# Optimization experiments

Hardware: AMD Instinct MI355X
Metric: run time of the kernel (lower is better)

Reference implementation:

```python
import jax, jax.numpy as jnp
import numpy as np

B, N, S, F0, C, NOUT = 16, 64, 4, 8, 32, 1
N_VALID = 48  # valid (unpadded) nodes per graph


def setup_inputs() -> dict:
    key = jax.random.key(0)
    ks = jax.random.split(key, 12)
    valid = (jnp.arange(N) < N_VALID).astype(jnp.float32)  # [N]
    # node features, zero for padded nodes; last column is the binary mask
    x_feat = jax.random.normal(ks[0], (B, N, F0), dtype=jnp.float32) * valid[None, :, None]
    x = jnp.concatenate([x_feat, jnp.broadcast_to(valid[None, :, None], (B, N, 1))], axis=-1)
    # sparse-ish binary adjacency (avg degree ~ 0.1*N), zeroed on padded rows/cols
    a = (jax.random.uniform(ks[1], (B, N, N)) < 0.1).astype(jnp.float32)
    a = a * valid[None, :, None] * valid[None, None, :]
    # edge features, only on existing edges
    e = jax.random.normal(ks[2], (B, N, N, S), dtype=jnp.float32) * a[..., None]
    sc = 0.1
    return {
        "x": x, "a": a, "e": e,
        # ECCConv 1: F_in = F0 -> C
        "w1_kern": jax.random.normal(ks[3], (S, C * F0), dtype=jnp.float32) * sc,
        "b1_kern": jnp.zeros((C * F0,), jnp.float32),
        "w1_root": jax.random.normal(ks[4], (F0, C), dtype=jnp.float32) * sc,
        "b1": jnp.zeros((C,), jnp.float32),
        # ECCConv 2: F_in = C -> C
        "w2_kern": jax.random.normal(ks[5], (S, C * C), dtype=jnp.float32) * sc,
        "b2_kern": jnp.zeros((C * C,), jnp.float32),
        "w2_root": jax.random.normal(ks[6], (C, C), dtype=jnp.float32) * sc,
        "b2": jnp.zeros((C,), jnp.float32),
        # readout dense
        "w_dense": jax.random.normal(ks[7], (C, NOUT), dtype=jnp.float32) * sc,
        "b_dense": jnp.zeros((NOUT,), jnp.float32),
    }


def _ecc(x, a, e, wk, bk, wr, b, mask):
    # spektral ECCConv, batch mode
    Bb, Nn = x.shape[0], x.shape[1]
    Fin = x.shape[-1]
    Cc = wr.shape[1]
    # per-edge filter weights from edge features: [B,N,N,C,Fin]
    kernel = (e @ wk + bk).reshape(Bb, Nn, Nn, Cc, Fin)
    # output[b,t,c] = sum_{i,f} kernel[b,t,i,c,f] * a[b,t,i] * x[b,i,f]
    msg = jnp.einsum("btixy,bti,biy->btx", kernel, a, x)
    out = msg + x @ wr + b
    out = out * mask[..., None]  # keras mask applied before activation
    return jax.nn.relu(out)


def reference(x, a, e, w1_kern, b1_kern, w1_root, b1,
              w2_kern, b2_kern, w2_root, b2, w_dense, b_dense):
    # GraphMasking: strip last feature column, use it as node mask
    mask = x[..., -1]      # [B,N]
    h = x[..., :-1]        # [B,N,F0]
    h = _ecc(h, a, e, w1_kern, b1_kern, w1_root, b1, mask)
    h = _ecc(h, a, e, w2_kern, b2_kern, w2_root, b2, mask)
    pooled = jnp.sum(h * mask[..., None], axis=1)  # GlobalSumPool with mask -> [B,C]
    return pooled @ w_dense + b_dense              # [B, n_out]
```

## Files before the change

### kernel.cpp

```cpp
#include <hip/hip_runtime.h>
#include <hip/hip_bf16.h>

#define NT 1024

constexpr int B_ = 16, N_ = 64, S_ = 4, F0_ = 8, C_ = 32;
constexpr int MAXE = 32;

typedef __attribute__((ext_vector_type(8))) short short8;
typedef __attribute__((ext_vector_type(4))) float f32x4;

__device__ __forceinline__ unsigned short f2bf(float x) {
    __hip_bfloat16 h = __float2bfloat16(x);
    return *reinterpret_cast<unsigned short*>(&h);
}

template<int F, int LOG2F, int SFP, int KSTEPS>
__device__ __forceinline__ void ecc_layer(
    int tid, const float* hin, float* hout,
    const float* __restrict__ wk, const float* __restrict__ bk,
    const float* __restrict__ wr, const float* __restrict__ bb,
    const float4* ec4, const unsigned char* nbr_idx, const int* nbr_cnt,
    const float* mask_sh, unsigned short* u_bf, unsigned short* wT,
    float* b_sh)
{
    constexpr int SF = 6 * F;
    constexpr int KTOT = KSTEPS * 32;

    for (int idx = tid; idx < C_ * SF; idx += NT) {
        int c = idx / SF, sf = idx - c * SF;
        int s = sf / F, f = sf - s * F;
        float v;
        if (s < 4)       v = wk[(s * C_ + c) * F + f];
        else if (s == 4) v = bk[c * F + f];
        else             v = wr[f * C_ + c];
        wT[c * SFP + sf] = f2bf(v);
    }
    if (KTOT > SF) {
        constexpr int PADK = KTOT - SF;
        for (int idx = tid; idx < C_ * PADK; idx += NT) {
            int c = idx / PADK, k = idx - c * PADK;
            wT[c * SFP + SF + k] = 0;
        }
        for (int idx = tid; idx < N_ * PADK; idx += NT) {
            int t = idx / PADK, k = idx - t * PADK;
            u_bf[t * SFP + SF + k] = 0;
        }
    }
    if (tid < C_) b_sh[tid] = bb[tid];

    for (int pair = tid; pair < N_ * F; pair += NT) {
        int t = pair >> LOG2F;
        int f = pair & (F - 1);
        float u0 = 0.f, u1 = 0.f, u2 = 0.f, u3 = 0.f, u4 = 0.f;
        const int cnt = nbr_cnt[t];
        for (int j = 0; j < cnt; ++j) {
            int i = nbr_idx[t * MAXE + j];
            float hv = hin[i * F + f];
            float4 ev = ec4[t * MAXE + j];
            u0 = fmaf(ev.x, hv, u0);
            u1 = fmaf(ev.y, hv, u1);
            u2 = fmaf(ev.z, hv, u2);
            u3 = fmaf(ev.w, hv, u3);
            u4 += hv;
        }
        unsigned short* ut = u_bf + t * SFP;
        ut[0 * F + f] = f2bf(u0);
        ut[1 * F + f] = f2bf(u1);
        ut[2 * F + f] = f2bf(u2);
        ut[3 * F + f] = f2bf(u3);
        ut[4 * F + f] = f2bf(u4);
        ut[5 * F + f] = f2bf(hin[t * F + f]);
    }
    __syncthreads();

    const int wv = tid >> 6;
    if (wv < 8) {
        const int lane = tid & 63, quad = lane >> 4, l16 = lane & 15;
        const int mt = wv >> 1, nt = wv & 1;
        f32x4 acc = {0.f, 0.f, 0.f, 0.f};
        const unsigned short* arow = u_bf + (mt * 16 + l16) * SFP;
        const unsigned short* brow = wT + (nt * 16 + l16) * SFP;
#pragma unroll
        for (int kk = 0; kk < KSTEPS; ++kk) {
            const int kb = kk * 32 + quad * 8;
            short8 av = *reinterpret_cast<const short8*>(arow + kb);
            short8 bv = *reinterpret_cast<const short8*>(brow + kb);
            acc = __builtin_amdgcn_mfma_f32_16x16x32_bf16(av, bv, acc, 0, 0, 0);
        }
        const int cc = nt * 16 + l16;
        const float bc = b_sh[cc];
#pragma unroll
        for (int r = 0; r < 4; ++r) {
            const int tt = mt * 16 + quad * 4 + r;
            float v = (acc[r] + bc) * mask_sh[tt];
            hout[tt * C_ + cc] = v > 0.f ? v : 0.f;
        }
    }
    __syncthreads();
}

__global__ __launch_bounds__(NT) void ecc_fused(
    const float* __restrict__ x,  const float* __restrict__ a,  const float* __restrict__ e,
    const float* __restrict__ w1k, const float* __restrict__ b1k,
    const float* __restrict__ w1r, const float* __restrict__ b1v,
    const float* __restrict__ w2k, const float* __restrict__ b2k,
    const float* __restrict__ w2r, const float* __restrict__ b2v,
    const float* __restrict__ wd,  const float* __restrict__ bd,
    float* __restrict__ out)
{
    __shared__ float x_sh[N_ * F0_];
    __shared__ float mask_sh[N_];
    __shared__ float h_sh[N_ * C_];
    __shared__ __align__(16) unsigned short u_bf[N_ * 200];
    __shared__ __align__(16) unsigned short wT_bf[C_ * 200];
    __shared__ __align__(16) float4 ec4[N_ * MAXE];
    __shared__ unsigned char nbr_idx[N_ * MAXE];
    __shared__ int nbr_cnt[N_];
    __shared__ float b_sh[C_];
    __shared__ float wd_sh[C_];
    __shared__ float red_sh[NT / 64];

    const int b   = blockIdx.x;
    const int tid = threadIdx.x;
    const float* eb  = e + (size_t)b * N_ * N_ * S_;
    const float* a_g = a + (size_t)b * N_ * N_;

    for (int idx = tid; idx < N_ * (F0_ + 1); idx += NT) {
        int t = idx / 9, j = idx - t * 9;
        float v = x[(b * N_ + t) * 9 + j];
        if (j == F0_) mask_sh[t] = v;
        else          x_sh[t * F0_ + j] = v;
    }
    if (tid < C_) wd_sh[tid] = wd[tid];

    {
        const int wv = tid >> 6, lane = tid & 63;
        float av[4];
#pragma unroll
        for (int r = 0; r < 4; ++r) av[r] = a_g[(wv * 4 + r) * N_ + lane];
#pragma unroll
        for (int r = 0; r < 4; ++r) {
            const int t = wv * 4 + r;
            const unsigned long long m = __ballot(av[r] != 0.f);
            if (lane == 0) {
                int cnt = (int)__popcll(m);
                nbr_cnt[t] = cnt > MAXE ? MAXE : cnt;
            }
            if (av[r] != 0.f) {
                int pos = (int)__popcll(m & ((1ull << lane) - 1ull));
                if (pos < MAXE) {
                    nbr_idx[t * MAXE + pos] = (unsigned char)lane;
                    ec4[t * MAXE + pos] =
                        *reinterpret_cast<const float4*>(eb + (size_t)(t * N_ + lane) * S_);
                }
            }
        }
    }
    __syncthreads();

    ecc_layer<8, 3, 72, 2>(tid, x_sh, h_sh, w1k, b1k, w1r, b1v,
                           ec4, nbr_idx, nbr_cnt, mask_sh, u_bf, wT_bf, b_sh);
    ecc_layer<32, 5, 200, 6>(tid, h_sh, h_sh, w2k, b2k, w2r, b2v,
                             ec4, nbr_idx, nbr_cnt, mask_sh, u_bf, wT_bf, b_sh);

    float partial = 0.f;
    for (int oi = tid; oi < N_ * C_; oi += NT) {
        int t = oi >> 5, c = oi & 31;
        partial += h_sh[oi] * mask_sh[t] * wd_sh[c];
    }
#pragma unroll
    for (int off = 32; off > 0; off >>= 1)
        partial += __shfl_down(partial, off, 64);
    if ((tid & 63) == 0) red_sh[tid >> 6] = partial;
    __syncthreads();
    if (tid == 0) {
        float s = 0.f;
#pragma unroll
        for (int w = 0; w < NT / 64; ++w) s += red_sh[w];
        out[b] = s + bd[0];
    }
}

extern "C" void kernel_launch(void* const* d_in, const int* in_sizes, int n_in,
                              void* d_out, int out_size, void* d_ws, size_t ws_size,
                              hipStream_t stream) {
    ecc_fused<<<B_, NT, 0, stream>>>(
        (const float*)d_in[0],  (const float*)d_in[1],  (const float*)d_in[2],
        (const float*)d_in[3],  (const float*)d_in[4],  (const float*)d_in[5],
        (const float*)d_in[6],  (const float*)d_in[7],  (const float*)d_in[8],
        (const float*)d_in[9],  (const float*)d_in[10], (const float*)d_in[11],
        (const float*)d_in[12], (float*)d_out);
}
```

Baseline: 85.60 us.

## Hoist weight staging, prefetch edge features, fuse readout into layer-2 epilogue

Both layers' weight matrices are now staged into separate shared buffers in the prologue, alongside the adjacency and node loads, so their global latency overlaps instead of sitting between the two layers. Edge features for every candidate edge are loaded up front, together with the adjacency row, rather than only for existing edges after the ballot. This issues more memory traffic but lets more loads be in flight at once. The masked sum-pool and dense readout move into the layer-2 MFMA epilogue, which removes the write-back of the hidden states and the separate reduction loop, at the cost of extra shared memory for the duplicated buffers.

```diff
diff --git a/kernel.cpp b/kernel.cpp
--- a/kernel.cpp
+++ b/kernel.cpp
@@ -14,18 +14,12 @@
     return *reinterpret_cast<unsigned short*>(&h);
 }
 
-template<int F, int LOG2F, int SFP, int KSTEPS>
-__device__ __forceinline__ void ecc_layer(
-    int tid, const float* hin, float* hout,
-    const float* __restrict__ wk, const float* __restrict__ bk,
-    const float* __restrict__ wr, const float* __restrict__ bb,
-    const float4* ec4, const unsigned char* nbr_idx, const int* nbr_cnt,
-    const float* mask_sh, unsigned short* u_bf, unsigned short* wT,
-    float* b_sh)
-{
+template<int F, int SFP>
+__device__ __forceinline__ void stage_w(int tid, const float* __restrict__ wk,
+                                        const float* __restrict__ bk,
+                                        const float* __restrict__ wr,
+                                        unsigned short* wT) {
     constexpr int SF = 6 * F;
-    constexpr int KTOT = KSTEPS * 32;
-
     for (int idx = tid; idx < C_ * SF; idx += NT) {
         int c = idx / SF, sf = idx - c * SF;
         int s = sf / F, f = sf - s * F;
@@ -35,19 +29,14 @@
         else             v = wr[f * C_ + c];
         wT[c * SFP + sf] = f2bf(v);
     }
-    if (KTOT > SF) {
-        constexpr int PADK = KTOT - SF;
-        for (int idx = tid; idx < C_ * PADK; idx += NT) {
-            int c = idx / PADK, k = idx - c * PADK;
-            wT[c * SFP + SF + k] = 0;
-        }
-        for (int idx = tid; idx < N_ * PADK; idx += NT) {
-            int t = idx / PADK, k = idx - t * PADK;
-            u_bf[t * SFP + SF + k] = 0;
-        }
-    }
-    if (tid < C_) b_sh[tid] = bb[tid];
-
+}
+
+template<int F, int LOG2F, int SFP>
+__device__ __forceinline__ void u_phase(int tid, const float* hin,
+                                        const float4* ec4,
+                                        const unsigned char* nbr_idx,
+                                        const int* nbr_cnt,
+                                        unsigned short* u_bf) {
     for (int pair = tid; pair < N_ * F; pair += NT) {
         int t = pair >> LOG2F;
         int f = pair & (F - 1);
@@ -71,32 +60,24 @@
         ut[4 * F + f] = f2bf(u4);
         ut[5 * F + f] = f2bf(hin[t * F + f]);
     }
-    __syncthreads();
-
-    const int wv = tid >> 6;
-    if (wv < 8) {
-        const int lane = tid & 63, quad = lane >> 4, l16 = lane & 15;
-        const int mt = wv >> 1, nt = wv & 1;
-        f32x4 acc = {0.f, 0.f, 0.f, 0.f};
-        const unsigned short* arow = u_bf + (mt * 16 + l16) * SFP;
-        const unsigned short* brow = wT + (nt * 16 + l16) * SFP;
-#pragma unroll
-        for (int kk = 0; kk < KSTEPS; ++kk) {
-            const int kb = kk * 32 + quad * 8;
-            short8 av = *reinterpret_cast<const short8*>(arow + kb);
-            short8 bv = *reinterpret_cast<const short8*>(brow + kb);
-            acc = __builtin_amdgcn_mfma_f32_16x16x32_bf16(av, bv, acc, 0, 0, 0);
-        }
-        const int cc = nt * 16 + l16;
-        const float bc = b_sh[cc];
-#pragma unroll
-        for (int r = 0; r < 4; ++r) {
-            const int tt = mt * 16 + quad * 4 + r;
-            float v = (acc[r] + bc) * mask_sh[tt];
-            hout[tt * C_ + cc] = v > 0.f ? v : 0.f;
-        }
-    }
-    __syncthreads();
+}
+
+template<int SFP, int KSTEPS>
+__device__ __forceinline__ f32x4 mfma_tile(int lane, int mt, int nt,
+                                           const unsigned short* u_bf,
+                                           const unsigned short* wT) {
+    const int quad = lane >> 4, l16 = lane & 15;
+    f32x4 acc = {0.f, 0.f, 0.f, 0.f};
+    const unsigned short* arow = u_bf + (mt * 16 + l16) * SFP;
+    const unsigned short* brow = wT + (nt * 16 + l16) * SFP;
+#pragma unroll
+    for (int kk = 0; kk < KSTEPS; ++kk) {
+        const int kb = kk * 32 + quad * 8;
+        short8 av = *reinterpret_cast<const short8*>(arow + kb);
+        short8 bv = *reinterpret_cast<const short8*>(brow + kb);
+        acc = __builtin_amdgcn_mfma_f32_16x16x32_bf16(av, bv, acc, 0, 0, 0);
+    }
+    return acc;
 }
 
 __global__ __launch_bounds__(NT) void ecc_fused(
@@ -111,33 +92,31 @@
     __shared__ float x_sh[N_ * F0_];
     __shared__ float mask_sh[N_];
     __shared__ float h_sh[N_ * C_];
-    __shared__ __align__(16) unsigned short u_bf[N_ * 200];
-    __shared__ __align__(16) unsigned short wT_bf[C_ * 200];
+    __shared__ __align__(16) unsigned short u1_bf[N_ * 72];
+    __shared__ __align__(16) unsigned short u2_bf[N_ * 200];
+    __shared__ __align__(16) unsigned short wT1[C_ * 72];
+    __shared__ __align__(16) unsigned short wT2[C_ * 200];
     __shared__ __align__(16) float4 ec4[N_ * MAXE];
     __shared__ unsigned char nbr_idx[N_ * MAXE];
     __shared__ int nbr_cnt[N_];
-    __shared__ float b_sh[C_];
-    __shared__ float wd_sh[C_];
-    __shared__ float red_sh[NT / 64];
+    __shared__ float b1_sh[C_], b2_sh[C_], wd_sh[C_];
+    __shared__ float red_sh[8];
 
     const int b   = blockIdx.x;
     const int tid = threadIdx.x;
     const float* eb  = e + (size_t)b * N_ * N_ * S_;
     const float* a_g = a + (size_t)b * N_ * N_;
 
-    for (int idx = tid; idx < N_ * (F0_ + 1); idx += NT) {
-        int t = idx / 9, j = idx - t * 9;
-        float v = x[(b * N_ + t) * 9 + j];
-        if (j == F0_) mask_sh[t] = v;
-        else          x_sh[t * F0_ + j] = v;
-    }
-    if (tid < C_) wd_sh[tid] = wd[tid];
-
     {
         const int wv = tid >> 6, lane = tid & 63;
-        float av[4];
-#pragma unroll
-        for (int r = 0; r < 4; ++r) av[r] = a_g[(wv * 4 + r) * N_ + lane];
+        float  av[4];
+        float4 ev[4];
+#pragma unroll
+        for (int r = 0; r < 4; ++r) {
+            const int t = wv * 4 + r;
+            av[r] = a_g[t * N_ + lane];
+            ev[r] = *reinterpret_cast<const float4*>(eb + (size_t)(t * N_ + lane) * S_);
+        }
 #pragma unroll
         for (int r = 0; r < 4; ++r) {
             const int t = wv * 4 + r;
@@ -150,34 +129,79 @@
                 int pos = (int)__popcll(m & ((1ull << lane) - 1ull));
                 if (pos < MAXE) {
                     nbr_idx[t * MAXE + pos] = (unsigned char)lane;
-                    ec4[t * MAXE + pos] =
-                        *reinterpret_cast<const float4*>(eb + (size_t)(t * N_ + lane) * S_);
+                    ec4[t * MAXE + pos] = ev[r];
                 }
             }
         }
     }
-    __syncthreads();
-
-    ecc_layer<8, 3, 72, 2>(tid, x_sh, h_sh, w1k, b1k, w1r, b1v,
-                           ec4, nbr_idx, nbr_cnt, mask_sh, u_bf, wT_bf, b_sh);
-    ecc_layer<32, 5, 200, 6>(tid, h_sh, h_sh, w2k, b2k, w2r, b2v,
-                             ec4, nbr_idx, nbr_cnt, mask_sh, u_bf, wT_bf, b_sh);
-
-    float partial = 0.f;
-    for (int oi = tid; oi < N_ * C_; oi += NT) {
-        int t = oi >> 5, c = oi & 31;
-        partial += h_sh[oi] * mask_sh[t] * wd_sh[c];
-    }
-#pragma unroll
-    for (int off = 32; off > 0; off >>= 1)
-        partial += __shfl_down(partial, off, 64);
-    if ((tid & 63) == 0) red_sh[tid >> 6] = partial;
+    for (int idx = tid; idx < N_ * (F0_ + 1); idx += NT) {
+        int t = idx / 9, j = idx - t * 9;
+        float v = x[(b * N_ + t) * 9 + j];
+        if (j == F0_) mask_sh[t] = v;
+        else          x_sh[t * F0_ + j] = v;
+    }
+    stage_w<8, 72>(tid, w1k, b1k, w1r, wT1);
+    stage_w<32, 200>(tid, w2k, b2k, w2r, wT2);
+    if (tid < C_) { b1_sh[tid] = b1v[tid]; b2_sh[tid] = b2v[tid]; wd_sh[tid] = wd[tid]; }
+    for (int idx = tid; idx < (N_ + C_) * 16; idx += NT) {
+        int row = idx >> 4, k = idx & 15;
+        if (row < N_) u1_bf[row * 72 + 48 + k] = 0;
+        else          wT1[(row - N_) * 72 + 48 + k] = 0;
+    }
+    __syncthreads();
+
+    u_phase<8, 3, 72>(tid, x_sh, ec4, nbr_idx, nbr_cnt, u1_bf);
+    __syncthreads();
+
+    {
+        const int wv = tid >> 6;
+        if (wv < 8) {
+            const int lane = tid & 63, quad = lane >> 4, l16 = lane & 15;
+            const int mt = wv >> 1, nt = wv & 1;
+            f32x4 acc = mfma_tile<72, 2>(lane, mt, nt, u1_bf, wT1);
+            const int cc = nt * 16 + l16;
+            const float bc = b1_sh[cc];
+#pragma unroll
+            for (int r = 0; r < 4; ++r) {
+                const int tt = mt * 16 + quad * 4 + r;
+                float v = (acc[r] + bc) * mask_sh[tt];
+                h_sh[tt * C_ + cc] = v > 0.f ? v : 0.f;
+            }
+        }
+    }
+    __syncthreads();
+
+    u_phase<32, 5, 200>(tid, h_sh, ec4, nbr_idx, nbr_cnt, u2_bf);
+    __syncthreads();
+
+    {
+        const int wv = tid >> 6;
+        float partial = 0.f;
+        if (wv < 8) {
+            const int lane = tid & 63, quad = lane >> 4, l16 = lane & 15;
+            const int mt = wv >> 1, nt = wv & 1;
+            f32x4 acc = mfma_tile<200, 6>(lane, mt, nt, u2_bf, wT2);
+            const int cc = nt * 16 + l16;
+            const float bc = b2_sh[cc];
+            const float wc = wd_sh[cc];
+#pragma unroll
+            for (int r = 0; r < 4; ++r) {
+                const int tt = mt * 16 + quad * 4 + r;
+                float v = (acc[r] + bc) * mask_sh[tt];
+                partial += (v > 0.f ? v : 0.f) * wc;
+            }
+#pragma unroll
+            for (int off = 32; off > 0; off >>= 1)
+                partial += __shfl_down(partial, off, 64);
+            if (lane == 0) red_sh[wv] = partial;
+        }
+    }
     __syncthreads();
     if (tid == 0) {
-        float s = 0.f;
-#pragma unroll
-        for (int w = 0; w < NT / 64; ++w) s += red_sh[w];
-        out[b] = s + bd[0];
+        float s = bd[0];
+#pragma unroll
+        for (int w = 0; w < 8; ++w) s += red_sh[w];
+        out[b] = s;
     }
 }
 
```

After: 87.12 us. Within noise of the previous version (+1.8%).
